# Performance work log

Measured on AMD Instinct MI355X. Metric: run time of the kernel, lower is better.

The kernel has to match this reference:

```python
import jax, jax.numpy as jnp
import numpy as np

VOCAB = 32000
H = 256        # d_model
L = 4096       # l_max
N = 64         # SSM state size (S4 default)
CH = 1         # channels
BATCH = 8
PAD = 0        # pad_token_id
DT_MIN, DT_MAX = 0.001, 0.1


def setup_inputs() -> dict:
    key = jax.random.key(0)
    ks = jax.random.split(key, 8)
    input_ids = jax.random.randint(ks[0], (BATCH, L), 0, VOCAB)
    embedding = (jax.random.normal(ks[1], (VOCAB, H), dtype=jnp.float32) * 0.02).at[PAD].set(0.0)
    # S4D-Lin style initialization
    log_dt = jnp.log(DT_MIN) + jax.random.uniform(ks[2], (H,), dtype=jnp.float32) * (np.log(DT_MAX) - np.log(DT_MIN))
    A_log_re = jnp.full((H, N), np.log(0.5), dtype=jnp.float32)          # A_real = -exp(A_log_re)
    A_im = jnp.broadcast_to(np.pi * jnp.arange(N, dtype=jnp.float32), (H, N)).copy()
    B_re = jnp.ones((H, N), dtype=jnp.float32)
    B_im = jnp.zeros((H, N), dtype=jnp.float32)
    # bidirectional => 2*CH output channels for C
    C_re = jax.random.normal(ks[3], (2 * CH, H, N), dtype=jnp.float32) * (0.5 ** 0.5)
    C_im = jax.random.normal(ks[4], (2 * CH, H, N), dtype=jnp.float32) * (0.5 ** 0.5)
    D = jax.random.normal(ks[5], (CH, H), dtype=jnp.float32)
    W_out = jax.random.normal(ks[6], (2 * H, CH * H), dtype=jnp.float32) / np.sqrt(CH * H)
    b_out = jnp.zeros((2 * H,), dtype=jnp.float32)
    return {"input_ids": input_ids, "embedding": embedding, "log_dt": log_dt,
            "A_log_re": A_log_re, "A_im": A_im, "B_re": B_re, "B_im": B_im,
            "C_re": C_re, "C_im": C_im, "D": D, "W_out": W_out, "b_out": b_out}


def _s4_forward(input_ids, embedding, log_dt, A_log_re, A_im, B_re, B_im, C_re, C_im, D, W_out, b_out):
    u = embedding[input_ids]                 # (B, L, H) embedding lookup
    u = jnp.swapaxes(u, 1, 2)                # (B, H, L) transposed=True
    dt = jnp.exp(log_dt)                     # (H,)
    A = -jnp.exp(A_log_re) + 1j * A_im       # (H, N) Hurwitz diagonal SSM
    dtA = dt[:, None] * A                    # (H, N)
    dA = jnp.exp(dtA)                        # discrete A (ZOH)
    dB = (B_re + 1j * B_im) * (dA - 1.0) / A # discrete B (ZOH), (H, N)
    Cc = C_re + 1j * C_im                    # (2*CH, H, N)
    # Vandermonde kernel: K[c,h,l] = 2*Re(sum_n C[c,h,n] dB[h,n] exp(dtA[h,n]*l))
    pos = jnp.arange(L, dtype=jnp.float32)
    vand = jnp.exp(dtA[:, :, None] * pos)    # (H, N, L) complex
    K = 2.0 * jnp.einsum('chn,hn,hnl->chl', Cc, dB, vand).real  # (2*CH, H, L)
    # bidirectional: causal kernel + flipped anti-causal kernel, conv length 2L
    k0, k1 = K[:CH], K[CH:]
    k = jnp.pad(k0, ((0, 0), (0, 0), (0, L))) + jnp.pad(k1[..., ::-1], ((0, 0), (0, 0), (L, 0)))
    k_f = jnp.fft.rfft(k, n=2 * L)           # (CH, H, L+1)
    u_f = jnp.fft.rfft(u, n=2 * L)           # (B, H, L+1)
    y = jnp.fft.irfft(u_f[:, None] * k_f[None], n=2 * L)[..., :L]  # (B, CH, H, L)
    y = y + u[:, None, :, :] * D[None, :, :, None]                 # skip connection
    y = y.reshape(u.shape[0], CH * H, L)
    y = jax.nn.gelu(y, approximate=False)
    z = jnp.einsum('oi,bil->bol', W_out, y) + b_out[None, :, None]  # (B, 2H, L)
    y = z[:, :H] * jax.nn.sigmoid(z[:, H:])                          # GLU
    y = jnp.swapaxes(y, 1, 2)                # (B, L, H)
    return y[:, -1]                           # pool='last' -> (B, H)


def reference(input_ids, embedding, log_dt, A_log_re, A_im, B_re, B_im, C_re, C_im, D, W_out, b_out):
    return _s4_forward(input_ids, embedding, log_dt, A_log_re, A_im, B_re, B_im, C_re, C_im, D, W_out, b_out)
```

## Files before the change

### kernel.cpp

```cpp
#include <hip/hip_runtime.h>
#include <math.h>

#define HH 256
#define NN 64
#define LL 4096
#define BB 8
#define TK 32
#define NCH (LL / TK)


__global__ __launch_bounds__(512) void kmat_kernel(
    const float* __restrict__ log_dt, const float* __restrict__ A_log_re,
    const float* __restrict__ A_im, const float* __restrict__ B_re,
    const float* __restrict__ B_im, const float* __restrict__ C_re,
    const float* __restrict__ C_im, float* __restrict__ Ktrev,
    float* __restrict__ y) {
    __shared__ struct {
        float powR[64][65]; float powI[64][65];
        float2 dAt[64]; float2 e64t[64]; float2 W2[8][64];
    } sk;
    int t = threadIdx.x;
    int h = blockIdx.x;
    int w = __builtin_amdgcn_readfirstlane(t >> 6);
    int lane = t & 63;
    if (h == 0) {
        #pragma unroll
        for (int i = 0; i < BB * HH / 512; ++i) y[i * 512 + t] = 0.0f;
    }
    if (t < NN) {
        int n = t;
        int idx = h * NN + n;
        float dt = expf(log_dt[h]);
        float Are = -expf(A_log_re[idx]);
        float Aim = A_im[idx];
        float ea = expf(dt * Are);
        float sn, cs;
        sincosf(dt * Aim, &sn, &cs);
        float dAre = ea * cs, dAim = ea * sn;
        float numre = dAre - 1.0f, numim = dAim;
        float den = Are * Are + Aim * Aim;
        float qre = (numre * Are + numim * Aim) / den;
        float qim = (numim * Are - numre * Aim) / den;
        float bre = B_re[idx], bim = B_im[idx];
        float dBre = bre * qre - bim * qim;
        float dBim = bre * qim + bim * qre;
        float cre = C_re[idx], cim = C_im[idx];
        float wre = 2.0f * (cre * dBre - cim * dBim);
        float wim = 2.0f * (cre * dBim + cim * dBre);
        sk.dAt[n] = make_float2(dAre, dAim);
        float pr = dAre, pi = dAim;
        #pragma unroll
        for (int kq = 0; kq < 6; ++kq) {
            float nr = pr * pr - pi * pi;
            pi = 2.0f * pr * pi; pr = nr;
        }
        sk.e64t[n] = make_float2(pr, pi);
        #pragma unroll
        for (int kq = 0; kq < 3; ++kq) {
            float nr = pr * pr - pi * pi;
            pi = 2.0f * pr * pi; pr = nr;
        }
        float qr2 = wre, qi2 = wim;
        #pragma unroll
        for (int kk = 0; kk < 8; ++kk) {
            sk.W2[kk][n] = make_float2(qr2, qi2);
            float nr = qr2 * pr - qi2 * pi, ni = qr2 * pi + qi2 * pr;
            qr2 = nr; qi2 = ni;
        }
    }
    __syncthreads();
    {
        float2 a = sk.dAt[lane];
        float br = a.x, bi = a.y;
        #pragma unroll
        for (int kq = 0; kq < 3; ++kq) {
            float nr = br * br - bi * bi;
            bi = 2.0f * br * bi; br = nr;
        }
        float pr = 1.0f, pi = 0.0f;
        #pragma unroll
        for (int bit = 0; bit < 3; ++bit) {
            if ((w >> bit) & 1) {
                float tr = pr * br - pi * bi;
                pi = pr * bi + pi * br; pr = tr;
            }
            float t2 = br * br - bi * bi;
            bi = 2.0f * br * bi; br = t2;
        }
        #pragma unroll
        for (int i = 0; i < 8; ++i) {
            sk.powR[8 * w + i][lane] = pr;
            sk.powI[8 * w + i][lane] = pi;
            float tr = pr * a.x - pi * a.y;
            pi = pr * a.y + pi * a.x; pr = tr;
        }
    }
    __syncthreads();
    float kacc[8];
    #pragma unroll
    for (int j = 0; j < 8; ++j) kacc[j] = 0.0f;
    #pragma unroll 2
    for (int n = 0; n < NN; ++n) {
        float Pr = sk.powR[lane][n];
        float Pi = sk.powI[lane][n];
        float2 E = sk.e64t[n];
        float2 Wn = sk.W2[w][n];
        float vr = Wn.x * Pr - Wn.y * Pi;
        float vi = Wn.x * Pi + Wn.y * Pr;
        #pragma unroll
        for (int j = 0; j < 8; ++j) {
            kacc[j] += vr;
            float tr = vr * E.x - vi * E.y;
            vi = vr * E.y + vi * E.x; vr = tr;
        }
    }
    #pragma unroll
    for (int j = 0; j < 8; ++j) {
        int l = w * 512 + j * 64 + lane;
        Ktrev[(long)(LL - 1 - l) * HH + h] = kacc[j];
    }
}

__global__ __launch_bounds__(256) void gconv_kernel(
    const int* __restrict__ ids, const float* __restrict__ emb,
    const float* __restrict__ Ktrev, float* __restrict__ y) {
    __shared__ float Kls[TK * HH];
    __shared__ int idsl[TK];
    int t = threadIdx.x;
    int b = blockIdx.x >> 7;
    int c = blockIdx.x & (NCH - 1);
    int i0 = c * TK;
    int wv = t >> 6, lane = t & 63;
    if (t < TK) idsl[t] = ids[b * LL + i0 + t];
    {
        const float* src = Ktrev + (long)i0 * HH;
        #pragma unroll
        for (int r = 0; r < 8; ++r) {
            int row = wv * 8 + r;
            __builtin_amdgcn_global_load_lds(
                (const __attribute__((address_space(1))) void*)
                    (src + row * HH + lane * 4),
                (__attribute__((address_space(3))) void*)(&Kls[row * HH]),
                16, 0, 0);
        }
    }
    __syncthreads();
    float acc = 0.0f;
    #pragma unroll 8
    for (int l = 0; l < TK; ++l) {
        int id = idsl[l];
        float v = emb[(long)id * HH + t];
        acc = fmaf(v, Kls[l * HH + t], acc);
    }
    atomicAdd(&y[b * HH + t], acc);
}

__global__ __launch_bounds__(256) void out_kernel(
    const float* __restrict__ y, const int* __restrict__ ids,
    const float* __restrict__ emb, const float* __restrict__ Dv,
    const float* __restrict__ W, const float* __restrict__ bvec,
    float* __restrict__ out) {
    int b = blockIdx.x >> 7;
    int tile = blockIdx.x & 127;
    int t = threadIdx.x;
    int w = t >> 6, lane = t & 63;
    __shared__ float gs[HH];
    __shared__ float zb[4];
    int idl = ids[b * LL + LL - 1];
    float yv = y[b * HH + t] + emb[(long)idl * HH + t] * Dv[t];
    gs[t] = 0.5f * yv * (1.0f + erff(yv * 0.70710678118654752f));
    __syncthreads();
    int hh = tile * 2 + (w >> 1);
    int o = (w & 1) * HH + hh;
    float4 wv4 = ((const float4*)(W + o * HH))[lane];
    float4 gv4 = ((const float4*)gs)[lane];
    float p = wv4.x * gv4.x + wv4.y * gv4.y + wv4.z * gv4.z + wv4.w * gv4.w;
    #pragma unroll
    for (int m = 32; m > 0; m >>= 1) p += __shfl_xor(p, m);
    if (lane == 0) zb[w] = p + bvec[o];
    __syncthreads();
    if (t < 2) {
        int hq = tile * 2 + t;
        float z1 = zb[t * 2 + 0];
        float z2 = zb[t * 2 + 1];
        out[b * HH + hq] = z1 * (1.0f / (1.0f + expf(-z2)));
    }
}

extern "C" void kernel_launch(void* const* d_in, const int* in_sizes, int n_in,
                              void* d_out, int out_size, void* d_ws, size_t ws_size,
                              hipStream_t stream) {
    const int* input_ids = (const int*)d_in[0];
    const float* embedding = (const float*)d_in[1];
    const float* log_dt = (const float*)d_in[2];
    const float* A_log_re = (const float*)d_in[3];
    const float* A_im = (const float*)d_in[4];
    const float* B_re = (const float*)d_in[5];
    const float* B_im = (const float*)d_in[6];
    const float* C_re = (const float*)d_in[7];
    const float* C_im = (const float*)d_in[8];
    const float* D = (const float*)d_in[9];
    const float* W_out = (const float*)d_in[10];
    const float* b_out = (const float*)d_in[11];
    float* out = (float*)d_out;

    float* ws = (float*)d_ws;
    float* Ktrev = ws;
    float* y = ws + 1048576;

    kmat_kernel<<<HH, 512, 0, stream>>>(
        log_dt, A_log_re, A_im, B_re, B_im, C_re, C_im, Ktrev, y);

    gconv_kernel<<<BB * NCH, 256, 0, stream>>>(
        input_ids, embedding, Ktrev, y);

    out_kernel<<<BB * 128, 256, 0, stream>>>(
        y, input_ids, embedding, D, W_out, b_out, out);
}
```

Before: 122.4 us.

## Fuse output projection into gconv via last-block ticket counter

Removes the separate out_kernel launch. Each gconv block takes a per-batch atomic ticket, and the last block to finish for a batch reads the accumulated y, applies the skip term and GELU, and computes the full 512-row W_out projection plus the GLU. This saves a kernel launch and its dependency gap, but puts the whole projection for a batch on a single block of 4 waves doing 128 dot products each, which serialises work that used to be spread over 1024 blocks.

```diff
diff --git a/kernel.cpp b/kernel.cpp
--- a/kernel.cpp
+++ b/kernel.cpp
@@ -14,7 +14,7 @@
     const float* __restrict__ A_im, const float* __restrict__ B_re,
     const float* __restrict__ B_im, const float* __restrict__ C_re,
     const float* __restrict__ C_im, float* __restrict__ Ktrev,
-    float* __restrict__ y) {
+    float* __restrict__ y, int* __restrict__ ticket) {
     __shared__ struct {
         float powR[64][65]; float powI[64][65];
         float2 dAt[64]; float2 e64t[64]; float2 W2[8][64];
@@ -26,6 +26,7 @@
     if (h == 0) {
         #pragma unroll
         for (int i = 0; i < BB * HH / 512; ++i) y[i * 512 + t] = 0.0f;
+        if (t < BB) ticket[t] = 0;
     }
     if (t < NN) {
         int n = t;
@@ -123,9 +124,15 @@
 
 __global__ __launch_bounds__(256) void gconv_kernel(
     const int* __restrict__ ids, const float* __restrict__ emb,
-    const float* __restrict__ Ktrev, float* __restrict__ y) {
+    const float* __restrict__ Ktrev, float* __restrict__ y,
+    int* __restrict__ ticket, const float* __restrict__ Dv,
+    const float* __restrict__ W, const float* __restrict__ bvec,
+    float* __restrict__ out) {
     __shared__ float Kls[TK * HH];
     __shared__ int idsl[TK];
+    __shared__ float gs[HH];
+    __shared__ float zbuf[2 * HH];
+    __shared__ int role;
     int t = threadIdx.x;
     int b = blockIdx.x >> 7;
     int c = blockIdx.x & (NCH - 1);
@@ -153,38 +160,36 @@
         acc = fmaf(v, Kls[l * HH + t], acc);
     }
     atomicAdd(&y[b * HH + t], acc);
-}
-
-__global__ __launch_bounds__(256) void out_kernel(
-    const float* __restrict__ y, const int* __restrict__ ids,
-    const float* __restrict__ emb, const float* __restrict__ Dv,
-    const float* __restrict__ W, const float* __restrict__ bvec,
-    float* __restrict__ out) {
-    int b = blockIdx.x >> 7;
-    int tile = blockIdx.x & 127;
-    int t = threadIdx.x;
-    int w = t >> 6, lane = t & 63;
-    __shared__ float gs[HH];
-    __shared__ float zb[4];
-    int idl = ids[b * LL + LL - 1];
-    float yv = y[b * HH + t] + emb[(long)idl * HH + t] * Dv[t];
+    asm volatile("s_waitcnt vmcnt(0)" ::: "memory");
+    __syncthreads();
+    if (t == 0) {
+        int old = atomicAdd(&ticket[b], 1);
+        role = (old == NCH - 1);
+    }
+    __syncthreads();
+    if (!role) return;
+
+    int idl = idsl[TK - 1];
+    if (c != NCH - 1) idl = ids[b * LL + LL - 1];
+    float yv = __hip_atomic_load(&y[b * HH + t], __ATOMIC_RELAXED,
+                                 __HIP_MEMORY_SCOPE_AGENT);
+    yv += emb[(long)idl * HH + t] * Dv[t];
     gs[t] = 0.5f * yv * (1.0f + erff(yv * 0.70710678118654752f));
     __syncthreads();
-    int hh = tile * 2 + (w >> 1);
-    int o = (w & 1) * HH + hh;
-    float4 wv4 = ((const float4*)(W + o * HH))[lane];
-    float4 gv4 = ((const float4*)gs)[lane];
-    float p = wv4.x * gv4.x + wv4.y * gv4.y + wv4.z * gv4.z + wv4.w * gv4.w;
-    #pragma unroll
-    for (int m = 32; m > 0; m >>= 1) p += __shfl_xor(p, m);
-    if (lane == 0) zb[w] = p + bvec[o];
-    __syncthreads();
-    if (t < 2) {
-        int hq = tile * 2 + t;
-        float z1 = zb[t * 2 + 0];
-        float z2 = zb[t * 2 + 1];
-        out[b * HH + hq] = z1 * (1.0f / (1.0f + expf(-z2)));
-    }
+    float4 gr = ((const float4*)gs)[lane];
+    #pragma unroll 4
+    for (int oo = 0; oo < 128; ++oo) {
+        int o = wv * 128 + oo;
+        float4 wr = ((const float4*)(W + o * HH))[lane];
+        float p = wr.x * gr.x + wr.y * gr.y + wr.z * gr.z + wr.w * gr.w;
+        #pragma unroll
+        for (int m = 32; m > 0; m >>= 1) p += __shfl_xor(p, m);
+        if (lane == 0) zbuf[o] = p + bvec[o];
+    }
+    __syncthreads();
+    float z1 = zbuf[t];
+    float z2 = zbuf[t + HH];
+    out[b * HH + t] = z1 * (1.0f / (1.0f + expf(-z2)));
 }
 
 extern "C" void kernel_launch(void* const* d_in, const int* in_sizes, int n_in,
@@ -207,13 +212,11 @@
     float* ws = (float*)d_ws;
     float* Ktrev = ws;
     float* y = ws + 1048576;
+    int* ticket = (int*)(ws + 1050624);
 
     kmat_kernel<<<HH, 512, 0, stream>>>(
-        log_dt, A_log_re, A_im, B_re, B_im, C_re, C_im, Ktrev, y);
+        log_dt, A_log_re, A_im, B_re, B_im, C_re, C_im, Ktrev, y, ticket);
 
     gconv_kernel<<<BB * NCH, 256, 0, stream>>>(
-        input_ids, embedding, Ktrev, y);
-
-    out_kernel<<<BB * 128, 256, 0, stream>>>(
-        y, input_ids, embedding, D, W_out, b_out, out);
+        input_ids, embedding, Ktrev, y, ticket, D, W_out, b_out, out);
 }
```

Measured after the change: 198.7 us. 62.3% more time.

## Load K directly to registers in gconv, halve tile, fold D skip into gconv

Applied to the files above, without the earlier changes.

The gconv kernel no longer stages the K tile in LDS through global_load_lds plus a barrier. Each thread now loads its embedding values and K values straight into register arrays, with a sched_barrier so all loads are issued before the FMAs. TK drops from 32 to 16, doubling the block count and the number of atomicAdds. The D skip term is folded into the last chunk's block, which removes the embedding gather from out_kernel.

```diff
diff --git a/kernel.cpp b/kernel.cpp
--- a/kernel.cpp
+++ b/kernel.cpp
@@ -5,7 +5,7 @@
 #define NN 64
 #define LL 4096
 #define BB 8
-#define TK 32
+#define TK 16
 #define NCH (LL / TK)
 
 
@@ -123,51 +123,37 @@
 
 __global__ __launch_bounds__(256) void gconv_kernel(
     const int* __restrict__ ids, const float* __restrict__ emb,
-    const float* __restrict__ Ktrev, float* __restrict__ y) {
-    __shared__ float Kls[TK * HH];
-    __shared__ int idsl[TK];
+    const float* __restrict__ Ktrev, float* __restrict__ y,
+    const float* __restrict__ Dv) {
     int t = threadIdx.x;
-    int b = blockIdx.x >> 7;
+    int b = blockIdx.x >> 8;
     int c = blockIdx.x & (NCH - 1);
     int i0 = c * TK;
-    int wv = t >> 6, lane = t & 63;
-    if (t < TK) idsl[t] = ids[b * LL + i0 + t];
-    {
-        const float* src = Ktrev + (long)i0 * HH;
-        #pragma unroll
-        for (int r = 0; r < 8; ++r) {
-            int row = wv * 8 + r;
-            __builtin_amdgcn_global_load_lds(
-                (const __attribute__((address_space(1))) void*)
-                    (src + row * HH + lane * 4),
-                (__attribute__((address_space(3))) void*)(&Kls[row * HH]),
-                16, 0, 0);
-        }
-    }
-    __syncthreads();
+    const int* idp = ids + b * LL + i0;
+    float ve[TK], kv[TK];
+    #pragma unroll
+    for (int l = 0; l < TK; ++l) {
+        ve[l] = emb[(long)idp[l] * HH + t];
+        kv[l] = Ktrev[(long)(i0 + l) * HH + t];
+    }
+    __builtin_amdgcn_sched_barrier(0);
     float acc = 0.0f;
-    #pragma unroll 8
-    for (int l = 0; l < TK; ++l) {
-        int id = idsl[l];
-        float v = emb[(long)id * HH + t];
-        acc = fmaf(v, Kls[l * HH + t], acc);
-    }
+    #pragma unroll
+    for (int l = 0; l < TK; ++l) acc = fmaf(ve[l], kv[l], acc);
+    if (c == NCH - 1) acc = fmaf(ve[TK - 1], Dv[t], acc);
     atomicAdd(&y[b * HH + t], acc);
 }
 
 __global__ __launch_bounds__(256) void out_kernel(
-    const float* __restrict__ y, const int* __restrict__ ids,
-    const float* __restrict__ emb, const float* __restrict__ Dv,
-    const float* __restrict__ W, const float* __restrict__ bvec,
-    float* __restrict__ out) {
+    const float* __restrict__ y, const float* __restrict__ W,
+    const float* __restrict__ bvec, float* __restrict__ out) {
     int b = blockIdx.x >> 7;
     int tile = blockIdx.x & 127;
     int t = threadIdx.x;
     int w = t >> 6, lane = t & 63;
     __shared__ float gs[HH];
     __shared__ float zb[4];
-    int idl = ids[b * LL + LL - 1];
-    float yv = y[b * HH + t] + emb[(long)idl * HH + t] * Dv[t];
+    float yv = y[b * HH + t];
     gs[t] = 0.5f * yv * (1.0f + erff(yv * 0.70710678118654752f));
     __syncthreads();
     int hh = tile * 2 + (w >> 1);
@@ -212,8 +198,8 @@
         log_dt, A_log_re, A_im, B_re, B_im, C_re, C_im, Ktrev, y);
 
     gconv_kernel<<<BB * NCH, 256, 0, stream>>>(
-        input_ids, embedding, Ktrev, y);
+        input_ids, embedding, Ktrev, y, D);
 
     out_kernel<<<BB * 128, 256, 0, stream>>>(
-        y, input_ids, embedding, D, W_out, b_out, out);
-}
+        y, W_out, b_out, out);
+}
```

Result: slower. 128.9 us (+5.3%).
